# Performance work log

Measured on AMD Instinct MI355X. Metric: run time of the kernel, lower is better.

The kernel has to match this reference:

```python
import jax, jax.numpy as jnp
import numpy as np
import math

NB = 4           # num_bands
EPS = 1e-5       # LayerNorm eps


def _dwconv(x, w):
    # depthwise Conv1d, padding=1, kernel=3. x: [b, t, c], w: [c, 1, k]
    c = x.shape[-1]
    y = jax.lax.conv_general_dilated(
        x.transpose(0, 2, 1), w, window_strides=(1,), padding=[(1, 1)],
        dimension_numbers=('NCH', 'OIH', 'NCH'), feature_group_count=c)
    return y.transpose(0, 2, 1)


def _ln(x, g, b):
    m = jnp.mean(x, axis=-1, keepdims=True)
    v = jnp.mean(jnp.square(x - m), axis=-1, keepdims=True)
    return (x - m) * jax.lax.rsqrt(v + EPS) * g + b


def _attn(x, mem, qw, qc, kw, kc, vw, vc, ow, pw, prev_qk):
    # x, mem: [b, w, c]
    b, w, c = x.shape
    d = c // NB
    q = _dwconv(x @ qw.T, qc).reshape(b, w, NB, d).transpose(0, 2, 1, 3)      # [b,nb,w,d]
    k = _dwconv(mem @ kw.T, kc).reshape(b, w, NB, d).transpose(0, 2, 3, 1)    # [b,nb,d,w]
    v = _dwconv(mem @ vw.T, vc).reshape(b, w, NB, d).transpose(0, 2, 1, 3)    # [b,nb,w,d]
    # skewed relative-position bias: matmul + pad + transpose + slice
    p = jnp.einsum('bnwd,dt->bnwt', q, pw[:, :w])                              # [b,nb,w,w]
    p = jnp.pad(p, ((0, 0), (0, 0), (0, 0), (1, 0)))                           # pad last dim left
    p = p.transpose(0, 1, 3, 2)[:, :, 1:, :]                                   # skew
    qk = (jnp.einsum('bnwd,bndt->bnwt', q, k) + p) / math.sqrt(c)
    if prev_qk is not None:
        qk = qk + prev_qk
    a = jnp.einsum('bnwt,bntd->bnwd', jax.nn.softmax(qk, axis=-1), v)
    a = a.transpose(0, 2, 1, 3).reshape(b, w, c)
    return a @ ow.T, qk


def setup_inputs() -> dict:
    key = jax.random.key(0)
    ks = jax.random.split(key, 32)
    B, CH, BINS, W, FF = 4, 8, 1024, 1024, 2048
    s = 0.02
    inp = {
        'x': jax.random.normal(ks[0], (B, CH, BINS, W), jnp.float32),
        'mem': jax.random.normal(ks[1], (B, CH, BINS, W), jnp.float32),
        'prev_qk1': jax.random.normal(ks[2], (B, NB, W, W), jnp.float32),
        'prev_qk2': jax.random.normal(ks[3], (B, NB, W, W), jnp.float32),
        'ip_w': jax.random.normal(ks[4], (CH,), jnp.float32) * s,
        'ip_b': jnp.zeros((1,), jnp.float32),
        'mp_w': jax.random.normal(ks[5], (CH,), jnp.float32) * s,
        'mp_b': jnp.zeros((1,), jnp.float32),
        'ln1_g': jnp.ones((BINS,), jnp.float32), 'ln1_b': jnp.zeros((BINS,), jnp.float32),
        'ln2_g': jnp.ones((BINS,), jnp.float32), 'ln2_b': jnp.zeros((BINS,), jnp.float32),
        'ln3_g': jnp.ones((BINS,), jnp.float32), 'ln3_b': jnp.zeros((BINS,), jnp.float32),
        'a1_qw': jax.random.normal(ks[6], (BINS, BINS), jnp.float32) * s,
        'a1_qc': jax.random.normal(ks[7], (BINS, 1, 3), jnp.float32) * 0.3,
        'a1_kw': jax.random.normal(ks[8], (BINS, BINS), jnp.float32) * s,
        'a1_kc': jax.random.normal(ks[9], (BINS, 1, 3), jnp.float32) * 0.3,
        'a1_vw': jax.random.normal(ks[10], (BINS, BINS), jnp.float32) * s,
        'a1_vc': jax.random.normal(ks[11], (BINS, 1, 3), jnp.float32) * 0.3,
        'a1_ow': jax.random.normal(ks[12], (BINS, BINS), jnp.float32) * s,
        'a1_pw': jax.random.normal(ks[13], (BINS // NB, W), jnp.float32),
        'a2_qw': jax.random.normal(ks[14], (BINS, BINS), jnp.float32) * s,
        'a2_qc': jax.random.normal(ks[15], (BINS, 1, 3), jnp.float32) * 0.3,
        'a2_kw': jax.random.normal(ks[16], (BINS, BINS), jnp.float32) * s,
        'a2_kc': jax.random.normal(ks[17], (BINS, 1, 3), jnp.float32) * 0.3,
        'a2_vw': jax.random.normal(ks[18], (BINS, BINS), jnp.float32) * s,
        'a2_vc': jax.random.normal(ks[19], (BINS, 1, 3), jnp.float32) * 0.3,
        'a2_ow': jax.random.normal(ks[20], (BINS, BINS), jnp.float32) * s,
        'a2_pw': jax.random.normal(ks[21], (BINS // NB, W), jnp.float32),
        'l1_w': jax.random.normal(ks[22], (FF, BINS), jnp.float32) * s,
        'l2_w': jax.random.normal(ks[23], (BINS, FF), jnp.float32) * s,
    }
    return inp


def reference(x, mem, prev_qk1, prev_qk2, ip_w, ip_b, mp_w, mp_b,
              ln1_g, ln1_b, ln2_g, ln2_b, ln3_g, ln3_b,
              a1_qw, a1_qc, a1_kw, a1_kc, a1_vw, a1_vc, a1_ow, a1_pw,
              a2_qw, a2_qc, a2_kw, a2_kc, a2_vw, a2_vc, a2_ow, a2_pw,
              l1_w, l2_w):
    # 1x1 Conv2d to 1 channel then [b, w, bins] layout
    xs = jnp.einsum('bchw,c->bwh', x, ip_w) + ip_b    # [b, w, bins]
    ms = jnp.einsum('bchw,c->bwh', mem, mp_w) + mp_b
    # self-attention with prev_qk residual
    h, qk1 = _attn(_ln(xs, ln1_g, ln1_b), _ln(xs, ln1_g, ln1_b),
                   a1_qw, a1_qc, a1_kw, a1_kc, a1_vw, a1_vc, a1_ow, a1_pw, prev_qk1)
    xs = xs + h
    # cross-attention against mem
    h, qk2 = _attn(_ln(xs, ln2_g, ln2_b), ms,
                   a2_qw, a2_qc, a2_kw, a2_kc, a2_vw, a2_vc, a2_ow, a2_pw, prev_qk2)
    xs = xs + h
    # squared-ReLU FFN
    h = _ln(xs, ln3_g, ln3_b)
    h = jnp.square(jax.nn.relu(h @ l1_w.T)) @ l2_w.T
    xs = xs + h
    out = xs.transpose(0, 2, 1)[:, None]              # [b, 1, bins, w]
    return (out, qk1, qk2)
```

## Files before the change

### kernel.cpp

```cpp
#include <hip/hip_runtime.h>
#include <stdint.h>

typedef unsigned short u16;
typedef __bf16 bfv8 __attribute__((ext_vector_type(8)));
typedef float f32x4 __attribute__((ext_vector_type(4)));
typedef unsigned short u16x8 __attribute__((ext_vector_type(8)));

#define DI __device__ __forceinline__

DI u16 f2bf(float f) {
  union { float f; unsigned u; } c; c.f = f;
  unsigned r = c.u + 0x7FFFu + ((c.u >> 16) & 1u);
  return (u16)(r >> 16);
}
DI float bf2f(u16 b) {
  union { unsigned u; float f; } c; c.u = ((unsigned)b) << 16;
  return c.f;
}

enum { EPI_BF16 = 0, EPI_RELU2 = 1, EPI_ADDF32 = 2, EPI_QK = 3 };

#define GLDS(g, l)                                                              \
  __builtin_amdgcn_global_load_lds((const __attribute__((address_space(1))) void*)(g), \
                                   (__attribute__((address_space(3))) void*)(l), 16, 0, 0)

#define VMCNT_BAR(N)                                        \
  do {                                                      \
    asm volatile("s_waitcnt vmcnt(" #N ")" ::: "memory");   \
    __builtin_amdgcn_sched_barrier(0);                      \
    __builtin_amdgcn_s_barrier();                           \
    __builtin_amdgcn_sched_barrier(0);                      \
  } while (0)

#define BAR_ONLY()                                          \
  do {                                                      \
    __builtin_amdgcn_sched_barrier(0);                      \
    __builtin_amdgcn_s_barrier();                           \
    __builtin_amdgcn_sched_barrier(0);                      \
  } while (0)

template <int EPI, bool KSPLIT, int BN>
__global__ __launch_bounds__(512) void gemm256(
    const u16* __restrict__ Aq, const u16* __restrict__ Akv, int asplit,
    long a1q, long a1r, int lda1,
    const u16* __restrict__ A2, int lda2,
    const u16* __restrict__ B1, long b1q, long b1r, int ldb1,
    const u16* __restrict__ B2, long b2q, long b2r, int ldb2,
    int K, int ksp,
    void* __restrict__ Cv, long cq, long cr, int ldc,
    const float* __restrict__ extra, long eq, int lde,
    float scale)
{
  constexpr int NJ = BN / 64;
  constexpr int NBL = BN / 64;
  constexpr int SS = 8192 + BN * 64;
  constexpr int LPS = 2 + NBL;
  __shared__ __align__(16) u16 lds[3 * SS];
  const int tid = threadIdx.x;
  const int wid = tid >> 6, lane = tid & 63;

  const int gx = gridDim.x, gy = gridDim.y;
  const int nwg = gx * gy * (int)gridDim.z;
  const int flat = blockIdx.x + gx * (blockIdx.y + gy * blockIdx.z);
  const int q = nwg >> 3, r = nwg & 7;
  const int xcd = flat & 7, idx = flat >> 3;
  const int wg = (xcd < r ? xcd * (q + 1) : r * (q + 1) + (xcd - r) * q) + idx;
  const int bx = wg % gx;
  const int tmp = wg / gx;
  const int by = tmp % gy;
  const int bz = tmp / gy;

  const long zq = bz >> 2, zr = bz & 3;
  const int m0 = by * 128, n0 = bx * BN;
  const u16* Ab = ((n0 >= asplit) ? Akv : Aq) + zq * a1q + zr * a1r;
  const u16* Bb = B1 + zq * b1q + zr * b1r;
  const u16* B2b = KSPLIT ? (B2 + zq * b2q + zr * b2r) : (const u16*)nullptr;
  const int wm = (wid >> 2) * 64, wn = (wid & 3) * (BN / 4);
  const int fr = lane & 15, fq = lane >> 4;

  f32x4 acc[4][NJ];
#pragma unroll
  for (int i = 0; i < 4; ++i)
#pragma unroll
    for (int j = 0; j < NJ; ++j)
      acc[i][j] = (f32x4){0.f, 0.f, 0.f, 0.f};

  const int nt = K >> 6;

  auto STAGE = [&](int tt, int sb) {
    const int k0 = tt << 6;
    u16* Ld = &lds[sb * SS];
    const u16* Asrc; int la; const u16* Bsrc; int lb;
    if (!KSPLIT || k0 < ksp) { Asrc = Ab + k0; la = lda1; Bsrc = Bb + k0; lb = ldb1; }
    else { Asrc = A2 + (k0 - ksp); la = lda2; Bsrc = B2b + (k0 - ksp); lb = ldb2; }
#pragma unroll
    for (int l = 0; l < 2; ++l) {
      int idx2 = (l << 9) + tid;
      int row = idx2 >> 3;
      int sc = ((idx2 & 7) ^ (row & 7)) << 3;
      GLDS(Asrc + (size_t)(m0 + row) * la + sc,
           Ld + (((l << 3) + wid) << 9));
    }
#pragma unroll
    for (int l = 0; l < NBL; ++l) {
      int idx2 = (l << 9) + tid;
      int row = idx2 >> 3;
      int sc = ((idx2 & 7) ^ (row & 7)) << 3;
      GLDS(Bsrc + (size_t)(n0 + row) * lb + sc,
           Ld + 8192 + (((l << 3) + wid) << 9));
    }
  };

  auto COMPUTE = [&](int cb) {
    const u16* As = &lds[cb * SS];
    const u16* Bs = As + 8192;
#pragma unroll
    for (int ks = 0; ks < 2; ++ks) {
      bfv8 av[4];
#pragma unroll
      for (int i = 0; i < 4; ++i) {
        int ra = wm + i * 16 + fr;
        int ca = (((ks << 2) + fq) ^ (ra & 7)) << 3;
        av[i] = *(const bfv8*)&As[(ra << 6) + ca];
      }
#pragma unroll
      for (int nh = 0; nh < NJ / 2; ++nh) {
        bfv8 bv[2];
#pragma unroll
        for (int j = 0; j < 2; ++j) {
          int rb = wn + (nh << 5) + (j << 4) + fr;
          int cb2 = (((ks << 2) + fq) ^ (rb & 7)) << 3;
          bv[j] = *(const bfv8*)&Bs[(rb << 6) + cb2];
        }
        __builtin_amdgcn_s_setprio(1);
#pragma unroll
        for (int i = 0; i < 4; ++i) {
          acc[i][(nh << 1)] = __builtin_amdgcn_mfma_f32_16x16x32_bf16(av[i], bv[0], acc[i][(nh << 1)], 0, 0, 0);
          acc[i][(nh << 1) + 1] = __builtin_amdgcn_mfma_f32_16x16x32_bf16(av[i], bv[1], acc[i][(nh << 1) + 1], 0, 0, 0);
        }
        __builtin_amdgcn_s_setprio(0);
      }
    }
  };

  STAGE(0, 0);
  STAGE(1, 1);
  if constexpr (LPS == 6) VMCNT_BAR(6); else VMCNT_BAR(4);
  int cur = 0;
  for (int t = 0; t < nt; ++t) {
    if (t + 2 < nt) {
      int stg = cur + 2; if (stg >= 3) stg -= 3;
      STAGE(t + 2, stg);
      COMPUTE(cur);
      if constexpr (LPS == 6) VMCNT_BAR(6); else VMCNT_BAR(4);
    } else if (t + 1 < nt) {
      COMPUTE(cur);
      VMCNT_BAR(0);
    } else {
      COMPUTE(cur);
    }
    cur = (cur == 2) ? 0 : cur + 1;
  }

  if constexpr (EPI == EPI_BF16 || EPI == EPI_RELU2) {
    u16* Cb = (u16*)Cv + zq * cq + zr * cr;
#pragma unroll
    for (int i = 0; i < 4; ++i)
#pragma unroll
      for (int j = 0; j < NJ; ++j)
#pragma unroll
        for (int r2 = 0; r2 < 4; ++r2) {
          int row = m0 + wm + i * 16 + (fq << 2) + r2;
          int col = n0 + wn + j * 16 + fr;
          float v = acc[i][j][r2];
          if constexpr (EPI == EPI_RELU2) { v = fmaxf(v, 0.f); v = v * v; }
          Cb[(size_t)row * ldc + col] = f2bf(v);
        }
  } else if constexpr (EPI == EPI_ADDF32) {
    float* Cb = (float*)Cv + zq * cq + zr * cr;
#pragma unroll
    for (int i = 0; i < 4; ++i)
#pragma unroll
      for (int j = 0; j < NJ; ++j)
#pragma unroll
        for (int r2 = 0; r2 < 4; ++r2) {
          int row = m0 + wm + i * 16 + (fq << 2) + r2;
          int col = n0 + wn + j * 16 + fr;
          Cb[(size_t)row * ldc + col] += acc[i][j][r2];
        }
  } else {
    float* Cb = (float*)Cv + zq * cq + zr * cr;
    const float* Eb = extra + (size_t)bz * eq;
#pragma unroll
    for (int i = 0; i < 4; ++i)
#pragma unroll
      for (int j = 0; j < NJ; ++j)
#pragma unroll
        for (int r2 = 0; r2 < 4; ++r2) {
          int row = m0 + wm + i * 16 + (fq << 2) + r2;
          int col = n0 + wn + j * 16 + fr;
          Cb[(size_t)row * ldc + col] = acc[i][j][r2] * scale + Eb[(size_t)row * lde + col];
        }
  }
}

__global__ __launch_bounds__(256) void proj4_kernel(const float* __restrict__ x,
                                                    const float* __restrict__ memp,
                                                    const float* __restrict__ ipw,
                                                    const float* __restrict__ ipb,
                                                    const float* __restrict__ mpw,
                                                    const float* __restrict__ mpb,
                                                    float* __restrict__ xs,
                                                    u16* __restrict__ msb)
{
  __shared__ __align__(16) float sbuf[2][16][256];
  const int t = threadIdx.x;
  const int wid = t >> 6, lane = t & 63;
  const int task = blockIdx.z >> 2;
  const int b = blockIdx.z & 3;
  const int h0 = blockIdx.x << 4;
  const int w0 = blockIdx.y << 8;
  const float* src = task ? memp : x;
  const float* w8 = task ? mpw : ipw;
  const float bias = task ? mpb[0] : ipb[0];
  const int crot = (blockIdx.x + blockIdx.y + blockIdx.z) & 7;
  float wr[8];
#pragma unroll
  for (int j = 0; j < 8; ++j) wr[j] = w8[(j + crot) & 7];
  float acc[16];
#pragma unroll
  for (int h = 0; h < 16; ++h) acc[h] = bias;
  const size_t bbase = ((size_t)b * 8) << 20;

  auto STAGE_C = [&](int i, int sb) {
    const int c = (i + crot) & 7;
    const float* g = src + bbase + ((size_t)c << 20) + (size_t)h0 * 1024 + w0 + (lane << 2);
#pragma unroll
    for (int l = 0; l < 4; ++l) {
      int row = (wid << 2) + l;
      GLDS(g + (size_t)row * 1024, &sbuf[sb][row][0]);
    }
  };

  STAGE_C(0, 0);
  STAGE_C(1, 1);
#pragma unroll
  for (int i = 0; i < 8; ++i) {
    if (i < 7) VMCNT_BAR(4); else VMCNT_BAR(0);
    {
      const float wc = wr[i];
      const int sb = i & 1;
#pragma unroll
      for (int h = 0; h < 16; ++h)
        acc[h] += sbuf[sb][h][t] * wc;
    }
    BAR_ONLY();
    if (i + 2 < 8) STAGE_C(i + 2, i & 1);
  }

  if (task) {
    u16* d = &msb[((size_t)b * 1024 + w0 + t) * 1024 + h0];
    u16x8 o0, o1;
#pragma unroll
    for (int h = 0; h < 8; ++h) { o0[h] = f2bf(acc[h]); o1[h] = f2bf(acc[h + 8]); }
    *(u16x8*)&d[0] = o0;
    *(u16x8*)&d[8] = o1;
  } else {
    float* d = &xs[((size_t)b * 1024 + w0 + t) * 1024 + h0];
#pragma unroll
    for (int p = 0; p < 4; ++p) {
      f32x4 v = {acc[p * 4], acc[p * 4 + 1], acc[p * 4 + 2], acc[p * 4 + 3]};
      *(f32x4*)&d[p * 4] = v;
    }
  }
}

__global__ __launch_bounds__(256) void ln_kernel(const float* __restrict__ x,
                                                 const float* __restrict__ g,
                                                 const float* __restrict__ b,
                                                 u16* __restrict__ out)
{
  int row = blockIdx.x, tid = threadIdx.x;
  float4 v = ((const float4*)(x + (size_t)row * 1024))[tid];
  float s = v.x + v.y + v.z + v.w;
  float s2 = v.x * v.x + v.y * v.y + v.z * v.z + v.w * v.w;
#pragma unroll
  for (int o = 32; o; o >>= 1) { s += __shfl_down(s, o); s2 += __shfl_down(s2, o); }
  __shared__ float rs[4], rs2[4];
  int wid = tid >> 6, lane = tid & 63;
  if (lane == 0) { rs[wid] = s; rs2[wid] = s2; }
  __syncthreads();
  s = rs[0] + rs[1] + rs[2] + rs[3];
  s2 = rs2[0] + rs2[1] + rs2[2] + rs2[3];
  float mean = s * (1.f / 1024.f);
  float var = s2 * (1.f / 1024.f) - mean * mean;
  float rstd = rsqrtf(var + 1e-5f);
  float4 gv = ((const float4*)g)[tid];
  float4 bv = ((const float4*)b)[tid];
  ushort4 o;
  o.x = f2bf((v.x - mean) * rstd * gv.x + bv.x);
  o.y = f2bf((v.y - mean) * rstd * gv.y + bv.y);
  o.z = f2bf((v.z - mean) * rstd * gv.z + bv.z);
  o.w = f2bf((v.w - mean) * rstd * gv.w + bv.w);
  ((ushort4*)out)[(size_t)row * 256 + tid] = o;
}

__global__ __launch_bounds__(128) void dwconv_qk_kernel(const u16* __restrict__ qkv,
                                                        const float* __restrict__ qc,
                                                        const float* __restrict__ kc,
                                                        u16* __restrict__ Qc,
                                                        u16* __restrict__ Kc)
{
  int sel = blockIdx.y;
  int row = blockIdx.x;
  int t = row & 1023;
  int c0 = threadIdx.x * 8;
  const u16* r0 = qkv + (size_t)row * 3072 + (sel << 10) + c0;
  const float* wc = sel ? kc : qc;
  u16* dst = (sel ? Kc : Qc) + (size_t)row * 1024 + c0;
  u16x8 zv = {0, 0, 0, 0, 0, 0, 0, 0};
  u16x8 xm = zv, xp = zv;
  if (t > 0) xm = *(const u16x8*)(r0 - 3072);
  u16x8 xc = *(const u16x8*)r0;
  if (t < 1023) xp = *(const u16x8*)(r0 + 3072);
  u16x8 o;
#pragma unroll
  for (int j = 0; j < 8; ++j) {
    int c = c0 + j;
    float v = bf2f(xm[j]) * wc[c * 3 + 0] + bf2f(xc[j]) * wc[c * 3 + 1] + bf2f(xp[j]) * wc[c * 3 + 2];
    o[j] = f2bf(v);
  }
  *(u16x8*)dst = o;
}

__global__ __launch_bounds__(1024) void dwconv_t_kernel(const u16* __restrict__ qkv,
                                                        const float* __restrict__ wc,
                                                        u16* __restrict__ out)
{
  __shared__ float tile[32][33];
  int b = blockIdx.z;
  int t = blockIdx.x * 32 + threadIdx.y;
  int c = blockIdx.y * 32 + threadIdx.x;
  size_t base = ((size_t)b * 1024 + t) * 3072 + 2048 + c;
  float xm = (t > 0) ? bf2f(qkv[base - 3072]) : 0.f;
  float xc = bf2f(qkv[base]);
  float xp = (t < 1023) ? bf2f(qkv[base + 3072]) : 0.f;
  tile[threadIdx.y][threadIdx.x] = xm * wc[c * 3 + 0] + xc * wc[c * 3 + 1] + xp * wc[c * 3 + 2];
  __syncthreads();
  int c2 = blockIdx.y * 32 + threadIdx.y;
  int t2 = blockIdx.x * 32 + threadIdx.x;
  int z = b * 4 + (c2 >> 8);
  out[((size_t)z * 256 + (c2 & 255)) * 1024 + t2] = f2bf(tile[threadIdx.x][threadIdx.y]);
}

__global__ __launch_bounds__(256) void softmax_kernel(const float* __restrict__ qk,
                                                      u16* __restrict__ P)
{
  size_t row = blockIdx.x;
  int tid = threadIdx.x;
  float4 v = ((const float4*)(qk + row * 1024))[tid];
  float m = fmaxf(fmaxf(v.x, v.y), fmaxf(v.z, v.w));
#pragma unroll
  for (int o = 32; o; o >>= 1) m = fmaxf(m, __shfl_down(m, o));
  __shared__ float red[4];
  int wid = tid >> 6, lane = tid & 63;
  if (lane == 0) red[wid] = m;
  __syncthreads();
  m = fmaxf(fmaxf(red[0], red[1]), fmaxf(red[2], red[3]));
  float e0 = __expf(v.x - m), e1 = __expf(v.y - m), e2 = __expf(v.z - m), e3 = __expf(v.w - m);
  float s = e0 + e1 + e2 + e3;
#pragma unroll
  for (int o = 32; o; o >>= 1) s += __shfl_down(s, o);
  __syncthreads();
  if (lane == 0) red[wid] = s;
  __syncthreads();
  s = red[0] + red[1] + red[2] + red[3];
  float rinv = 1.f / s;
  ushort4 o;
  o.x = f2bf(e0 * rinv); o.y = f2bf(e1 * rinv); o.z = f2bf(e2 * rinv); o.w = f2bf(e3 * rinv);
  ((ushort4*)P)[row * 256 + tid] = o;
}

struct CastJobs { const float* s[12]; u16* d[12]; };
__global__ __launch_bounds__(256) void cast12_kernel(CastJobs J)
{
  int j = blockIdx.y;
  int i = blockIdx.x * 256 + threadIdx.x;
  float4 v = ((const float4*)J.s[j])[i];
  ushort4 o;
  o.x = f2bf(v.x); o.y = f2bf(v.y); o.z = f2bf(v.z); o.w = f2bf(v.w);
  ((ushort4*)J.d[j])[i] = o;
}

__global__ __launch_bounds__(1024) void pwt_kernel(const float* __restrict__ pw,
                                                   u16* __restrict__ pwT)
{
  __shared__ float tile[32][33];
  int d = blockIdx.y * 32 + threadIdx.y;
  int t = blockIdx.x * 32 + threadIdx.x;
  tile[threadIdx.y][threadIdx.x] = pw[(size_t)d * 1024 + t];
  __syncthreads();
  int t2 = blockIdx.x * 32 + threadIdx.y;
  int d2 = blockIdx.y * 32 + threadIdx.x;
  pwT[(size_t)t2 * 256 + d2] = f2bf(tile[threadIdx.x][threadIdx.y]);
}

__global__ __launch_bounds__(1024) void tout_kernel(const float* __restrict__ xs,
                                                    float* __restrict__ out)
{
  __shared__ float tile[32][33];
  int b = blockIdx.z;
  int w = blockIdx.x * 32 + threadIdx.y;
  int h = blockIdx.y * 32 + threadIdx.x;
  tile[threadIdx.y][threadIdx.x] = xs[((size_t)b * 1024 + w) * 1024 + h];
  __syncthreads();
  int h2 = blockIdx.y * 32 + threadIdx.y;
  int w2 = blockIdx.x * 32 + threadIdx.x;
  out[((size_t)b * 1024 + h2) * 1024 + w2] = tile[threadIdx.x][threadIdx.y];
}

static void run_attn(hipStream_t stream, float* xs, const u16* qsrc, const u16* kvsrc, int asplit,
                     u16* QKVraw, u16* Qc, u16* Kc, u16* Vt, u16* P, u16* Am,
                     const u16* wqkv, const u16* wo, const u16* pwt,
                     const float* qc, const float* kc, const float* vc,
                     const float* prevqk, float* qko)
{
  dim3 blk(512);
  gemm256<EPI_BF16, false, 256><<<dim3(12, 32, 1), blk, 0, stream>>>(
      qsrc, kvsrc, asplit, 0, 0, 1024, nullptr, 0,
      wqkv, 0, 0, 1024, nullptr, 0, 0, 0,
      1024, 0, QKVraw, 0, 0, 3072, nullptr, 0, 0, 1.f);
  dwconv_qk_kernel<<<dim3(4096, 2), 128, 0, stream>>>(QKVraw, qc, kc, Qc, Kc);
  dwconv_t_kernel<<<dim3(32, 32, 4), dim3(32, 32), 0, stream>>>(QKVraw, vc, Vt);
  gemm256<EPI_QK, true, 256><<<dim3(4, 8, 16), blk, 0, stream>>>(
      Qc, Qc, 1 << 30, 1048576, 256, 1024, pwt, 256,
      Kc, 1048576, 256, 1024, Qc, 1048576, 256, 1024,
      512, 256, qko, 4194304, 1048576, 1024, prevqk, 1048576, 1024, 0.03125f);
  softmax_kernel<<<16384, 256, 0, stream>>>(qko, P);
  gemm256<EPI_BF16, false, 128><<<dim3(2, 8, 16), blk, 0, stream>>>(
      P, P, 1 << 30, 4194304, 1048576, 1024, nullptr, 0,
      Vt, 1048576, 262144, 1024, nullptr, 0, 0, 0,
      1024, 0, Am, 1048576, 256, 1024, nullptr, 0, 0, 1.f);
  gemm256<EPI_ADDF32, false, 128><<<dim3(8, 32, 1), blk, 0, stream>>>(
      Am, Am, 1 << 30, 0, 0, 1024, nullptr, 0,
      wo, 0, 0, 1024, nullptr, 0, 0, 0,
      1024, 0, xs, 0, 0, 1024, nullptr, 0, 0, 1.f);
}

extern "C" void kernel_launch(void* const* d_in, const int* in_sizes, int n_in,
                              void* d_out, int out_size, void* d_ws, size_t ws_size,
                              hipStream_t stream)
{
  (void)in_sizes; (void)n_in; (void)out_size; (void)ws_size;
  const float* x    = (const float*)d_in[0];
  const float* memp = (const float*)d_in[1];
  const float* pqk1 = (const float*)d_in[2];
  const float* pqk2 = (const float*)d_in[3];
  const float* ip_w = (const float*)d_in[4];
  const float* ip_b = (const float*)d_in[5];
  const float* mp_w = (const float*)d_in[6];
  const float* mp_b = (const float*)d_in[7];
  const float* ln1g = (const float*)d_in[8];
  const float* ln1b = (const float*)d_in[9];
  const float* ln2g = (const float*)d_in[10];
  const float* ln2b = (const float*)d_in[11];
  const float* ln3g = (const float*)d_in[12];
  const float* ln3b = (const float*)d_in[13];
  const float* a1qw = (const float*)d_in[14];
  const float* a1qc = (const float*)d_in[15];
  const float* a1kw = (const float*)d_in[16];
  const float* a1kc = (const float*)d_in[17];
  const float* a1vw = (const float*)d_in[18];
  const float* a1vc = (const float*)d_in[19];
  const float* a1ow = (const float*)d_in[20];
  const float* a1pw = (const float*)d_in[21];
  const float* a2qw = (const float*)d_in[22];
  const float* a2qc = (const float*)d_in[23];
  const float* a2kw = (const float*)d_in[24];
  const float* a2kc = (const float*)d_in[25];
  const float* a2vw = (const float*)d_in[26];
  const float* a2vc = (const float*)d_in[27];
  const float* a2ow = (const float*)d_in[28];
  const float* a2pw = (const float*)d_in[29];
  const float* l1w  = (const float*)d_in[30];
  const float* l2w  = (const float*)d_in[31];

  float* outp = (float*)d_out;
  float* qk1o = outp + 4194304;
  float* qk2o = outp + 20971520;

  const size_t MB = 1024 * 1024;
  char* W = (char*)d_ws;
  float* xs   = (float*)(W);
  u16* msb    = (u16*)(W + 16 * MB);
  u16* xln    = (u16*)(W + 24 * MB);
  u16* QKVraw = (u16*)(W + 32 * MB);
  u16* Qc     = (u16*)(W + 56 * MB);
  u16* Kc     = (u16*)(W + 64 * MB);
  u16* Vt     = (u16*)(W + 72 * MB);
  u16* P      = (u16*)(W + 80 * MB);
  u16* Am     = (u16*)(W + 112 * MB);
  u16* wqkv1  = (u16*)(W + 120 * MB);
  u16* wqkv2  = (u16*)(W + 126 * MB);
  u16* wo1    = (u16*)(W + 132 * MB);
  u16* wo2    = (u16*)(W + 134 * MB);
  u16* wl1    = (u16*)(W + 136 * MB);
  u16* wl2    = (u16*)(W + 140 * MB);
  u16* pwt1   = (u16*)(W + 144 * MB);
  u16* pwt2   = (u16*)(W + 144 * MB + 512 * 1024);
  u16* H1     = QKVraw;

  CastJobs J;
  J.s[0] = a1qw; J.d[0] = wqkv1;
  J.s[1] = a1kw; J.d[1] = wqkv1 + 1048576;
  J.s[2] = a1vw; J.d[2] = wqkv1 + 2097152;
  J.s[3] = a2qw; J.d[3] = wqkv2;
  J.s[4] = a2kw; J.d[4] = wqkv2 + 1048576;
  J.s[5] = a2vw; J.d[5] = wqkv2 + 2097152;
  J.s[6] = a1ow; J.d[6] = wo1;
  J.s[7] = a2ow; J.d[7] = wo2;
  J.s[8] = l1w;            J.d[8] = wl1;
  J.s[9] = l1w + 1048576;  J.d[9] = wl1 + 1048576;
  J.s[10] = l2w;           J.d[10] = wl2;
  J.s[11] = l2w + 1048576; J.d[11] = wl2 + 1048576;
  cast12_kernel<<<dim3(1024, 12), 256, 0, stream>>>(J);
  pwt_kernel<<<dim3(32, 8, 1), dim3(32, 32), 0, stream>>>(a1pw, pwt1);
  pwt_kernel<<<dim3(32, 8, 1), dim3(32, 32), 0, stream>>>(a2pw, pwt2);

  proj4_kernel<<<dim3(64, 4, 8), 256, 0, stream>>>(
      x, memp, ip_w, ip_b, mp_w, mp_b, xs, msb);

  ln_kernel<<<4096, 256, 0, stream>>>(xs, ln1g, ln1b, xln);
  run_attn(stream, xs, xln, xln, 1 << 30, QKVraw, Qc, Kc, Vt, P, Am,
           wqkv1, wo1, pwt1, a1qc, a1kc, a1vc, pqk1, qk1o);

  ln_kernel<<<4096, 256, 0, stream>>>(xs, ln2g, ln2b, xln);
  run_attn(stream, xs, xln, msb, 1024, QKVraw, Qc, Kc, Vt, P, Am,
           wqkv2, wo2, pwt2, a2qc, a2kc, a2vc, pqk2, qk2o);

  ln_kernel<<<4096, 256, 0, stream>>>(xs, ln3g, ln3b, xln);
  gemm256<EPI_RELU2, false, 256><<<dim3(8, 32, 1), dim3(512), 0, stream>>>(
      xln, xln, 1 << 30, 0, 0, 1024, nullptr, 0,
      wl1, 0, 0, 1024, nullptr, 0, 0, 0,
      1024, 0, H1, 0, 0, 2048, nullptr, 0, 0, 1.f);
  gemm256<EPI_ADDF32, false, 128><<<dim3(8, 32, 1), dim3(512), 0, stream>>>(
      H1, H1, 1 << 30, 0, 0, 2048, nullptr, 0,
      wl2, 0, 0, 2048, nullptr, 0, 0, 0,
      2048, 0, xs, 0, 0, 1024, nullptr, 0, 0, 1.f);

  tout_kernel<<<dim3(32, 32, 4), dim3(32, 32), 0, stream>>>(xs, outp);
}
```

Baseline: 503.1 us.

## Replace 256-wide triple-buffered GEMM with 128x128 double-buffered occupancy-4 GEMM

Drops the BN template and makes every GEMM use a 128x128 tile with a 2-stage LDS ring instead of 3 stages. It adds __launch_bounds__(512,4) so more workgroups can be resident per CU. Grids for the QKV, QK and FFN1 GEMMs are doubled along N to match. The loop now computes, barriers, then issues the next stage. This gives up some per-block reuse of A tiles and overlap depth in return for more parallel blocks and less LDS and register pressure. The extra barrier and the register cap could cause spills or stalls.

```diff
diff --git a/kernel.cpp b/kernel.cpp
--- a/kernel.cpp
+++ b/kernel.cpp
@@ -39,8 +39,8 @@
     __builtin_amdgcn_sched_barrier(0);                      \
   } while (0)
 
-template <int EPI, bool KSPLIT, int BN>
-__global__ __launch_bounds__(512) void gemm256(
+template <int EPI, bool KSPLIT>
+__global__ __launch_bounds__(512, 4) void gemm128(
     const u16* __restrict__ Aq, const u16* __restrict__ Akv, int asplit,
     long a1q, long a1r, int lda1,
     const u16* __restrict__ A2, int lda2,
@@ -51,11 +51,9 @@
     const float* __restrict__ extra, long eq, int lde,
     float scale)
 {
-  constexpr int NJ = BN / 64;
-  constexpr int NBL = BN / 64;
-  constexpr int SS = 8192 + BN * 64;
-  constexpr int LPS = 2 + NBL;
-  __shared__ __align__(16) u16 lds[3 * SS];
+  constexpr int NJ = 2;
+  constexpr int SS = 16384;
+  __shared__ __align__(16) u16 lds[2 * SS];
   const int tid = threadIdx.x;
   const int wid = tid >> 6, lane = tid & 63;
 
@@ -71,11 +69,11 @@
   const int bz = tmp / gy;
 
   const long zq = bz >> 2, zr = bz & 3;
-  const int m0 = by * 128, n0 = bx * BN;
+  const int m0 = by * 128, n0 = bx * 128;
   const u16* Ab = ((n0 >= asplit) ? Akv : Aq) + zq * a1q + zr * a1r;
   const u16* Bb = B1 + zq * b1q + zr * b1r;
   const u16* B2b = KSPLIT ? (B2 + zq * b2q + zr * b2r) : (const u16*)nullptr;
-  const int wm = (wid >> 2) * 64, wn = (wid & 3) * (BN / 4);
+  const int wm = (wid >> 2) * 64, wn = (wid & 3) * 32;
   const int fr = lane & 15, fq = lane >> 4;
 
   f32x4 acc[4][NJ];
@@ -102,7 +100,7 @@
            Ld + (((l << 3) + wid) << 9));
     }
 #pragma unroll
-    for (int l = 0; l < NBL; ++l) {
+    for (int l = 0; l < 2; ++l) {
       int idx2 = (l << 9) + tid;
       int row = idx2 >> 3;
       int sc = ((idx2 & 7) ^ (row & 7)) << 3;
@@ -123,43 +121,35 @@
         int ca = (((ks << 2) + fq) ^ (ra & 7)) << 3;
         av[i] = *(const bfv8*)&As[(ra << 6) + ca];
       }
-#pragma unroll
-      for (int nh = 0; nh < NJ / 2; ++nh) {
-        bfv8 bv[2];
-#pragma unroll
-        for (int j = 0; j < 2; ++j) {
-          int rb = wn + (nh << 5) + (j << 4) + fr;
-          int cb2 = (((ks << 2) + fq) ^ (rb & 7)) << 3;
-          bv[j] = *(const bfv8*)&Bs[(rb << 6) + cb2];
-        }
-        __builtin_amdgcn_s_setprio(1);
-#pragma unroll
-        for (int i = 0; i < 4; ++i) {
-          acc[i][(nh << 1)] = __builtin_amdgcn_mfma_f32_16x16x32_bf16(av[i], bv[0], acc[i][(nh << 1)], 0, 0, 0);
-          acc[i][(nh << 1) + 1] = __builtin_amdgcn_mfma_f32_16x16x32_bf16(av[i], bv[1], acc[i][(nh << 1) + 1], 0, 0, 0);
-        }
-        __builtin_amdgcn_s_setprio(0);
+      bfv8 bv[2];
+#pragma unroll
+      for (int j = 0; j < 2; ++j) {
+        int rb = wn + (j << 4) + fr;
+        int cb2 = (((ks << 2) + fq) ^ (rb & 7)) << 3;
+        bv[j] = *(const bfv8*)&Bs[(rb << 6) + cb2];
       }
+      __builtin_amdgcn_s_setprio(1);
+#pragma unroll
+      for (int i = 0; i < 4; ++i) {
+        acc[i][0] = __builtin_amdgcn_mfma_f32_16x16x32_bf16(av[i], bv[0], acc[i][0], 0, 0, 0);
+        acc[i][1] = __builtin_amdgcn_mfma_f32_16x16x32_bf16(av[i], bv[1], acc[i][1], 0, 0, 0);
+      }
+      __builtin_amdgcn_s_setprio(0);
     }
   };
 
   STAGE(0, 0);
   STAGE(1, 1);
-  if constexpr (LPS == 6) VMCNT_BAR(6); else VMCNT_BAR(4);
-  int cur = 0;
+  VMCNT_BAR(4);
   for (int t = 0; t < nt; ++t) {
+    COMPUTE(t & 1);
+    BAR_ONLY();
     if (t + 2 < nt) {
-      int stg = cur + 2; if (stg >= 3) stg -= 3;
-      STAGE(t + 2, stg);
-      COMPUTE(cur);
-      if constexpr (LPS == 6) VMCNT_BAR(6); else VMCNT_BAR(4);
+      STAGE(t + 2, t & 1);
+      VMCNT_BAR(4);
     } else if (t + 1 < nt) {
-      COMPUTE(cur);
       VMCNT_BAR(0);
-    } else {
-      COMPUTE(cur);
-    }
-    cur = (cur == 2) ? 0 : cur + 1;
+    }
   }
 
   if constexpr (EPI == EPI_BF16 || EPI == EPI_RELU2) {
@@ -426,22 +416,22 @@
                      const float* prevqk, float* qko)
 {
   dim3 blk(512);
-  gemm256<EPI_BF16, false, 256><<<dim3(12, 32, 1), blk, 0, stream>>>(
+  gemm128<EPI_BF16, false><<<dim3(24, 32, 1), blk, 0, stream>>>(
       qsrc, kvsrc, asplit, 0, 0, 1024, nullptr, 0,
       wqkv, 0, 0, 1024, nullptr, 0, 0, 0,
       1024, 0, QKVraw, 0, 0, 3072, nullptr, 0, 0, 1.f);
   dwconv_qk_kernel<<<dim3(4096, 2), 128, 0, stream>>>(QKVraw, qc, kc, Qc, Kc);
   dwconv_t_kernel<<<dim3(32, 32, 4), dim3(32, 32), 0, stream>>>(QKVraw, vc, Vt);
-  gemm256<EPI_QK, true, 256><<<dim3(4, 8, 16), blk, 0, stream>>>(
+  gemm128<EPI_QK, true><<<dim3(8, 8, 16), blk, 0, stream>>>(
       Qc, Qc, 1 << 30, 1048576, 256, 1024, pwt, 256,
       Kc, 1048576, 256, 1024, Qc, 1048576, 256, 1024,
       512, 256, qko, 4194304, 1048576, 1024, prevqk, 1048576, 1024, 0.03125f);
   softmax_kernel<<<16384, 256, 0, stream>>>(qko, P);
-  gemm256<EPI_BF16, false, 128><<<dim3(2, 8, 16), blk, 0, stream>>>(
+  gemm128<EPI_BF16, false><<<dim3(2, 8, 16), blk, 0, stream>>>(
       P, P, 1 << 30, 4194304, 1048576, 1024, nullptr, 0,
       Vt, 1048576, 262144, 1024, nullptr, 0, 0, 0,
       1024, 0, Am, 1048576, 256, 1024, nullptr, 0, 0, 1.f);
-  gemm256<EPI_ADDF32, false, 128><<<dim3(8, 32, 1), blk, 0, stream>>>(
+  gemm128<EPI_ADDF32, false><<<dim3(8, 32, 1), blk, 0, stream>>>(
       Am, Am, 1 << 30, 0, 0, 1024, nullptr, 0,
       wo, 0, 0, 1024, nullptr, 0, 0, 0,
       1024, 0, xs, 0, 0, 1024, nullptr, 0, 0, 1.f);
@@ -539,11 +529,11 @@
            wqkv2, wo2, pwt2, a2qc, a2kc, a2vc, pqk2, qk2o);
 
   ln_kernel<<<4096, 256, 0, stream>>>(xs, ln3g, ln3b, xln);
-  gemm256<EPI_RELU2, false, 256><<<dim3(8, 32, 1), dim3(512), 0, stream>>>(
+  gemm128<EPI_RELU2, false><<<dim3(16, 32, 1), dim3(512), 0, stream>>>(
       xln, xln, 1 << 30, 0, 0, 1024, nullptr, 0,
       wl1, 0, 0, 1024, nullptr, 0, 0, 0,
       1024, 0, H1, 0, 0, 2048, nullptr, 0, 0, 1.f);
-  gemm256<EPI_ADDF32, false, 128><<<dim3(8, 32, 1), dim3(512), 0, stream>>>(
+  gemm128<EPI_ADDF32, false><<<dim3(8, 32, 1), dim3(512), 0, stream>>>(
       H1, H1, 1 << 30, 0, 0, 2048, nullptr, 0,
       wl2, 0, 0, 2048, nullptr, 0, 0, 0,
       2048, 0, xs, 0, 0, 1024, nullptr, 0, 0, 1.f);
```

Result: faster. 475.7 us (-5.4%).
